# Optimization experiments

Measured on AMD Instinct MI355X. Metric: run time of the kernel, lower is better.

## Reference

```python
import jax, jax.numpy as jnp
import numpy as np
from jax import lax

B, L_IN, D, D_INNER = 4, 1024, 512, 512
H, DK = 8, 64
WIN = [4, 4, 4]
INNER_SIZE = 5   # temporal intra-level neighborhood size
SEM_K = 32       # opt.semantic_node: topk per level for semantic mask
N_LAYER = 2


def _build_temporal_mask(input_size, window_size, inner_size):
    # faithful port of Encoder.get_mask (Pyraformer-Naive mask)
    all_size = [input_size]
    for w in window_size:
        all_size.append(all_size[-1] // w)
    L = sum(all_size)
    m = np.zeros((L, L), dtype=np.float32)
    iw = inner_size // 2
    starts = [sum(all_size[:i]) for i in range(len(all_size))]
    for li, n in enumerate(all_size):
        st = starts[li]
        for i in range(st, st + n):
            m[i, max(i - iw, st):min(i + iw + 1, st + n)] = 1
    for li in range(1, len(all_size)):
        st = starts[li]
        prev = all_size[li - 1]
        w = window_size[li - 1]
        for i in range(st, st + all_size[li]):
            ls = st - prev + (i - st) * w
            rs = st if i == st + all_size[li] - 1 else st - prev + (i - st + 1) * w
            m[i, ls:rs] = 1
            m[ls:rs, i] = 1
    return (1 - m).astype(bool), all_size

TMASK_NP, ALL_SIZE = _build_temporal_mask(L_IN, WIN, INNER_SIZE)
L_TOT = sum(ALL_SIZE)  # 1360


def _ln(x, g, b, eps):
    mu = jnp.mean(x, axis=-1, keepdims=True)
    var = jnp.mean(jnp.square(x - mu), axis=-1, keepdims=True)
    return (x - mu) * lax.rsqrt(var + eps) * g + b


def _mha(x, Wq, Wk, Wv, fcW, fcb, g, b, mask):
    # post-norm MHA (normalize_before=False), dropout disabled (eval)
    Bq, L, _ = x.shape
    q = (x @ Wq).reshape(Bq, L, H, DK)
    k = (x @ Wk).reshape(Bq, L, H, DK)
    v = (x @ Wv).reshape(Bq, L, H, DK)
    a = jnp.einsum('bqhd,bkhd->bhqk', q, k) / np.float32(DK ** 0.5)
    a = jnp.where(mask, -jnp.inf, a)
    p = jax.nn.softmax(a, axis=-1)
    o = jnp.einsum('bhqk,bkhd->bqhd', p, v).reshape(Bq, L, H * DK)
    return _ln(o @ fcW + fcb + x, g, b, 1e-6)


def _semantic_mask(x):
    # get_semantic_mask: per-level cosine similarity, mask topk-most-similar within each level
    nrm = jnp.linalg.norm(x, axis=-1, keepdims=True)
    xn = x / jnp.maximum(nrm, 1e-8)
    sim = jnp.einsum('bid,bjd->bij', xn, xn)
    Bq = x.shape[0]
    mask = jnp.zeros((Bq, L_TOT, L_TOT), dtype=bool)
    bidx = jnp.arange(Bq)[:, None, None]
    start = 0
    for n in ALL_SIZE:
        k = min(n, SEM_K)
        blk = sim[:, start:start + n, start:start + n]
        idx = lax.top_k(blk, k)[1]              # [B, n, k]
        ridx = jnp.arange(n)[None, :, None]
        bm = jnp.zeros((Bq, n, n), dtype=bool).at[bidx, ridx, idx].set(True)
        mask = mask.at[:, start:start + n, start:start + n].set(bm)
        start += n
    return mask


def _bottleneck(x, dW, db, cW, cb, uW, ub, g, b):
    t = jnp.transpose(x @ dW + db, (0, 2, 1))  # [B, d_inner, L]
    outs = []
    for i in range(len(WIN)):
        t = lax.conv_general_dilated(t, cW[i], (WIN[i],), 'VALID',
                                     dimension_numbers=('NCH', 'OIH', 'NCH')) + cb[i][None, :, None]
        t = t / np.float32(np.sqrt(1.0 + 1e-5))  # eval BatchNorm with identity running stats
        t = jax.nn.elu(t)
        outs.append(t)
    pyr = jnp.transpose(jnp.concatenate(outs, axis=2), (0, 2, 1)) @ uW + ub
    return _ln(jnp.concatenate([x, pyr], axis=1), g, b, 1e-5)


def _forward(x_enc, down_W, down_b, conv_W, conv_b, up_W, up_b, bc_ln_g, bc_ln_b,
             attn_Wq, attn_Wk, attn_Wv, attn_fcW, attn_fcb, attn_ln_g, attn_ln_b,
             ffn_W1, ffn_b1, ffn_W2, ffn_b2, ffn_ln_g, ffn_ln_b):
    tmask = jnp.asarray(TMASK_NP)[None, None]  # [1,1,Lt,Lt]
    x = _bottleneck(x_enc, down_W, down_b, conv_W, conv_b, up_W, up_b, bc_ln_g, bc_ln_b)
    for l in range(N_LAYER):
        res = x
        t_out = _mha(x, attn_Wq[l, 0], attn_Wk[l, 0], attn_Wv[l, 0], attn_fcW[l, 0],
                     attn_fcb[l, 0], attn_ln_g[l, 0], attn_ln_b[l, 0], tmask)
        smask = _semantic_mask(x)[:, None]     # [B,1,Lt,Lt]
        s_out = _mha(x, attn_Wq[l, 1], attn_Wk[l, 1], attn_Wv[l, 1], attn_fcW[l, 1],
                     attn_fcb[l, 1], attn_ln_g[l, 1], attn_ln_b[l, 1], smask)
        x = (t_out + s_out + res) / 3.0
        res = x
        h = jax.nn.relu(x @ ffn_W1[l] + ffn_b1[l])
        x = _ln(h @ ffn_W2[l] + ffn_b2[l] + res, ffn_ln_g[l], ffn_ln_b[l], 1e-6)
    return x


def setup_inputs() -> dict:
    key = jax.random.key(0)
    ks = jax.random.split(key, 16)
    s = 0.02
    inp = {
        'x_enc': jax.random.normal(ks[0], (B, L_IN, D), jnp.float32),
        'down_W': jax.random.normal(ks[1], (D, D_INNER), jnp.float32) * s,
        'down_b': jnp.zeros((D_INNER,), jnp.float32),
        'conv_W': jax.random.normal(ks[2], (3, D_INNER, D_INNER, WIN[0]), jnp.float32) * s,
        'conv_b': jnp.zeros((3, D_INNER), jnp.float32),
        'up_W': jax.random.normal(ks[3], (D_INNER, D), jnp.float32) * s,
        'up_b': jnp.zeros((D,), jnp.float32),
        'bc_ln_g': jnp.ones((D,), jnp.float32),
        'bc_ln_b': jnp.zeros((D,), jnp.float32),
        'attn_Wq': jax.random.normal(ks[4], (N_LAYER, 2, D, H * DK), jnp.float32) * s,
        'attn_Wk': jax.random.normal(ks[5], (N_LAYER, 2, D, H * DK), jnp.float32) * s,
        'attn_Wv': jax.random.normal(ks[6], (N_LAYER, 2, D, H * DK), jnp.float32) * s,
        'attn_fcW': jax.random.normal(ks[7], (N_LAYER, 2, H * DK, D), jnp.float32) * s,
        'attn_fcb': jnp.zeros((N_LAYER, 2, D), jnp.float32),
        'attn_ln_g': jnp.ones((N_LAYER, 2, D), jnp.float32),
        'attn_ln_b': jnp.zeros((N_LAYER, 2, D), jnp.float32),
        'ffn_W1': jax.random.normal(ks[8], (N_LAYER, D, D_INNER), jnp.float32) * s,
        'ffn_b1': jnp.zeros((N_LAYER, D_INNER), jnp.float32),
        'ffn_W2': jax.random.normal(ks[9], (N_LAYER, D_INNER, D), jnp.float32) * s,
        'ffn_b2': jnp.zeros((N_LAYER, D), jnp.float32),
        'ffn_ln_g': jnp.ones((N_LAYER, D), jnp.float32),
        'ffn_ln_b': jnp.zeros((N_LAYER, D), jnp.float32),
    }
    return inp


def reference(x_enc, down_W, down_b, conv_W, conv_b, up_W, up_b, bc_ln_g, bc_ln_b,
              attn_Wq, attn_Wk, attn_Wv, attn_fcW, attn_fcb, attn_ln_g, attn_ln_b,
              ffn_W1, ffn_b1, ffn_W2, ffn_b2, ffn_ln_g, ffn_ln_b):
    return _forward(x_enc, down_W, down_b, conv_W, conv_b, up_W, up_b, bc_ln_g, bc_ln_b,
                    attn_Wq, attn_Wk, attn_Wv, attn_fcW, attn_fcb, attn_ln_g, attn_ln_b,
                    ffn_W1, ffn_b1, ffn_W2, ffn_b2, ffn_ln_g, ffn_ln_b)
```

## Files before the change

### kernel.cpp

```cpp
#include <hip/hip_runtime.h>
#include <float.h>
#include <math.h>
#include <stdint.h>

#define LT 1360
#define BB 4
#define DM 512
#define NHH 8
#define NBLE 2785280
#define MBW 24
#define QSCALE 0.18033688f

typedef __attribute__((ext_vector_type(8))) short short8;
typedef __attribute__((ext_vector_type(4))) float f32x4;
typedef unsigned long long u64;

__device__ __forceinline__ ushort f2b(float x){
    uint32_t u = __float_as_uint(x);
    return (ushort)((u + 0x7fffu + ((u >> 16) & 1u)) >> 16);
}
__device__ __forceinline__ float b2f(ushort u){
    return __uint_as_float(((uint32_t)u) << 16);
}
__device__ __forceinline__ float ex2(float x){
    float r;
    asm("v_exp_f32 %0, %1" : "=v"(r) : "v"(x));
    return r;
}
__device__ __forceinline__ uint32_t pkbf(float lo, float hi){
    uint32_t r;
    asm("v_cvt_pk_bf16_f32 %0, %1, %2" : "=v"(r) : "v"(lo), "v"(hi));
    return r;
}

#define SG0 0
#define SG1 1048576
#define SG2 (SG1 + 65536)
#define SG3 (SG2 + 4096)
#define SBT (SG3 + 256)

__device__ __forceinline__ void blk_info(int i, int& bi, int& st, int& n){
    if (i < 1024){ bi = 0; st = 0;    n = 1024; }
    else if (i < 1280){ bi = 1; st = 1024; n = 256; }
    else if (i < 1344){ bi = 2; st = 1280; n = 64; }
    else { bi = 3; st = 1344; n = 16; }
}

__global__ __launch_bounds__(256)
void build_tidx(int* __restrict__ idx, int* __restrict__ cnt){
    int i = blockIdx.x * 256 + threadIdx.x;
    if (i >= LT) return;
    int bi, st, n; blk_info(i, bi, st, n);
    int c = 0; int* row = idx + i * 12;
    int lo = (i - 2 > st) ? i - 2 : st;
    int hi = (i + 2 < st + n - 1) ? i + 2 : st + n - 1;
    for (int j = lo; j <= hi; j++) row[c++] = j;
    if (bi < 3) row[c++] = st + n + (i - st) / 4;
    if (bi > 0){
        int stc = st - n * 4;
        int base = stc + (i - st) * 4;
        for (int t = 0; t < 4; t++) row[c++] = base + t;
    }
    cnt[i] = c;
    for (int t = c; t < 12; t++) row[t] = 0;
}

__global__ __launch_bounds__(256)
void wtrans(const float* __restrict__ W, ushort* __restrict__ Wt, int K, int N, long dstStride){
    int mat = blockIdx.z;
    const float* Ws = W + (size_t)mat * K * N;
    ushort* Wd = Wt + (size_t)mat * dstStride;
    int k0 = blockIdx.y << 6, n0 = blockIdx.x << 6;
    __shared__ ushort t[64][72];
    int tid = threadIdx.x;
    #pragma unroll
    for (int p = 0; p < 4; p++){
        int idx = tid + (p << 8);
        int r = idx >> 4, c4 = (idx & 15) << 2;
        float4 v = *(const float4*)(Ws + (size_t)(k0 + r) * N + n0 + c4);
        t[c4+0][r] = f2b(v.x); t[c4+1][r] = f2b(v.y);
        t[c4+2][r] = f2b(v.z); t[c4+3][r] = f2b(v.w);
    }
    __syncthreads();
    #pragma unroll
    for (int p = 0; p < 4; p++){
        int idx = tid + (p << 8);
        int r = idx >> 4, c4 = (idx & 15) << 2;
        *(uint2*)&Wd[(size_t)(n0 + r) * K + k0 + c4] = *(uint2*)&t[r][c4];
    }
}

__global__ __launch_bounds__(256)
void wconv(const float* __restrict__ cw, ushort* __restrict__ wt){
    int conv = blockIdx.y;
    const float* src = cw + (size_t)conv * 512 * 512 * 4;
    ushort* dst = wt + (size_t)conv * 2048 * 512;
    int idx = blockIdx.x * 256 + threadIdx.x;
    int o = idx >> 11, rest = idx & 2047;
    int k = rest >> 9, ii = rest & 511;
    dst[idx] = f2b(src[((size_t)(o << 9) + ii) * 4 + k]);
}

__global__ __launch_bounds__(256)
void gemm_qkv(const ushort* __restrict__ A, const ushort* __restrict__ Bw,
              void* __restrict__ Cout, int M, int N, int K)
{
    __shared__ ushort As[64][72];
    __shared__ ushort Bs[128][72];
    int tid = threadIdx.x;
    int lane = tid & 63, w = tid >> 6, quad = lane >> 4, l15 = lane & 15;
    int gm = blockIdx.y << 6, gn = blockIdx.x << 7;
    int arow = tid >> 2, ac = (tid & 3) << 4;
    int brow = tid >> 1, bc = (tid & 1) << 5;
    f32x4 acc[4][2];
    #pragma unroll
    for (int mi = 0; mi < 4; mi++)
        #pragma unroll
        for (int ni = 0; ni < 2; ni++)
            acc[mi][ni] = (f32x4){0.f,0.f,0.f,0.f};
    const ushort* Ap = A + (size_t)(gm + arow) * K + ac;
    const ushort* Bp = Bw + (size_t)(gn + brow) * K + bc;
    uint4 a0r = *(const uint4*)(Ap);
    uint4 a1r = *(const uint4*)(Ap + 8);
    uint4 b0r = *(const uint4*)(Bp);
    uint4 b1r = *(const uint4*)(Bp + 8);
    uint4 b2r = *(const uint4*)(Bp + 16);
    uint4 b3r = *(const uint4*)(Bp + 24);
    *(uint4*)&As[arow][ac]     = a0r;  *(uint4*)&As[arow][ac + 8]  = a1r;
    *(uint4*)&Bs[brow][bc]     = b0r;  *(uint4*)&Bs[brow][bc + 8]  = b1r;
    *(uint4*)&Bs[brow][bc + 16] = b2r; *(uint4*)&Bs[brow][bc + 24] = b3r;
    __syncthreads();
    for (int k0 = 0; k0 < K; k0 += 64){
        bool nx = (k0 + 64 < K);
        if (nx){
            a0r = *(const uint4*)(Ap + k0 + 64);
            a1r = *(const uint4*)(Ap + k0 + 72);
            b0r = *(const uint4*)(Bp + k0 + 64);
            b1r = *(const uint4*)(Bp + k0 + 72);
            b2r = *(const uint4*)(Bp + k0 + 80);
            b3r = *(const uint4*)(Bp + k0 + 88);
        }
        __builtin_amdgcn_s_setprio(1);
        #pragma unroll
        for (int kk = 0; kk < 2; kk++){
            short8 af[4], bf[2];
            #pragma unroll
            for (int mi = 0; mi < 4; mi++)
                af[mi] = *(const short8*)&As[(mi << 4) + l15][(kk << 5) + (quad << 3)];
            #pragma unroll
            for (int ni = 0; ni < 2; ni++)
                bf[ni] = *(const short8*)&Bs[(w << 5) + (ni << 4) + l15][(kk << 5) + (quad << 3)];
            #pragma unroll
            for (int mi = 0; mi < 4; mi++)
                #pragma unroll
                for (int ni = 0; ni < 2; ni++)
                    acc[mi][ni] = __builtin_amdgcn_mfma_f32_16x16x32_bf16(af[mi], bf[ni], acc[mi][ni], 0, 0, 0);
        }
        __builtin_amdgcn_s_setprio(0);
        if (nx){
            __syncthreads();
            *(uint4*)&As[arow][ac]     = a0r;  *(uint4*)&As[arow][ac + 8]  = a1r;
            *(uint4*)&Bs[brow][bc]     = b0r;  *(uint4*)&Bs[brow][bc + 8]  = b1r;
            *(uint4*)&Bs[brow][bc + 16] = b2r; *(uint4*)&Bs[brow][bc + 24] = b3r;
            __syncthreads();
        }
    }
    int seg = gn >> 9, gc = gn & 511;
    ushort* Ob = (ushort*)Cout;
    if (seg == 0){
        #pragma unroll
        for (int mi = 0; mi < 4; mi++)
            #pragma unroll
            for (int r = 0; r < 4; r++){
                int row = gm + (mi << 4) + (quad << 2) + r;
                #pragma unroll
                for (int ni = 0; ni < 2; ni++){
                    int c5 = gc + (w << 5) + (ni << 4) + l15;
                    Ob[(size_t)row * 512 + c5] = f2b(acc[mi][ni][r] * QSCALE);
                }
            }
    } else if (seg == 1){
        #pragma unroll
        for (int mi = 0; mi < 4; mi++)
            #pragma unroll
            for (int r = 0; r < 4; r++){
                int row = gm + (mi << 4) + (quad << 2) + r;
                #pragma unroll
                for (int ni = 0; ni < 2; ni++){
                    int c5 = gc + (w << 5) + (ni << 4) + l15;
                    Ob[(size_t)2*NBLE + (size_t)row * 512 + c5] = f2b(acc[mi][ni][r]);
                }
            }
    } else {
        __syncthreads();
        #pragma unroll
        for (int mi = 0; mi < 4; mi++)
            #pragma unroll
            for (int r = 0; r < 4; r++){
                int rloc = (mi << 4) + (quad << 2) + r;
                int row = gm + rloc;
                #pragma unroll
                for (int ni = 0; ni < 2; ni++){
                    int cloc = (w << 5) + (ni << 4) + l15;
                    ushort hv = f2b(acc[mi][ni][r]);
                    Ob[(size_t)5*NBLE + (size_t)row * 512 + gc + cloc] = hv;
                    Bs[cloc][rloc] = hv;
                }
            }
        __syncthreads();
        int colw = tid >> 3;
        int jo = (tid & 7) << 3;
        int rr = gm + jo;
        int bb = rr / LT;
        int ii = rr - bb * LT;
        #pragma unroll
        for (int cc = 0; cc < 4; cc++){
            int c = colw + (cc << 5);
            uint4 tv = *(const uint4*)&Bs[c][jo];
            ushort* dst = Ob + (size_t)4*NBLE + ((size_t)(bb * 512 + gc + c)) * LT + ii;
            *(uint4*)dst = tv;
        }
    }
}

template<int ABF>
__global__ __launch_bounds__(256)
void gemm64t(const void* __restrict__ Avp, const ushort* __restrict__ Bw,
             const float* __restrict__ bias, const float* __restrict__ Rres,
             void* __restrict__ Cout, int M, int N, int K,
             int act, int omode, int mpb, int orpb, int ooff)
{
    __shared__ ushort As[64][72];
    __shared__ ushort Bs[64][72];
    int tid = threadIdx.x;
    int lane = tid & 63, w = tid >> 6, quad = lane >> 4, l15 = lane & 15;
    int gm = blockIdx.y << 6, gn = blockIdx.x << 6;
    int wr = (w >> 1) << 5, wc = (w & 1) << 5;
    int srow = tid >> 2, sc = (tid & 3) << 4;
    f32x4 acc[2][2];
    #pragma unroll
    for (int mi = 0; mi < 2; mi++)
        #pragma unroll
        for (int ni = 0; ni < 2; ni++)
            acc[mi][ni] = (f32x4){0.f,0.f,0.f,0.f};
    const float*  Af = (const float*)Avp;
    const ushort* Ab = (const ushort*)Avp;
    size_t aoff = (size_t)(gm + srow) * K + sc;
    const ushort* Bp = Bw + (size_t)(gn + srow) * K + sc;
    uint4 aR0, aR1, bR0, bR1;
    float4 f0, f1, f2v, f3v;
    if (ABF){
        aR0 = *(const uint4*)(Ab + aoff);
        aR1 = *(const uint4*)(Ab + aoff + 8);
    } else {
        f0  = *(const float4*)(Af + aoff);
        f1  = *(const float4*)(Af + aoff + 4);
        f2v = *(const float4*)(Af + aoff + 8);
        f3v = *(const float4*)(Af + aoff + 12);
    }
    bR0 = *(const uint4*)(Bp);
    bR1 = *(const uint4*)(Bp + 8);
    if (!ABF){
        aR0.x = (uint32_t)f2b(f0.x)  | ((uint32_t)f2b(f0.y)  << 16);
        aR0.y = (uint32_t)f2b(f0.z)  | ((uint32_t)f2b(f0.w)  << 16);
        aR0.z = (uint32_t)f2b(f1.x)  | ((uint32_t)f2b(f1.y)  << 16);
        aR0.w = (uint32_t)f2b(f1.z)  | ((uint32_t)f2b(f1.w)  << 16);
        aR1.x = (uint32_t)f2b(f2v.x) | ((uint32_t)f2b(f2v.y) << 16);
        aR1.y = (uint32_t)f2b(f2v.z) | ((uint32_t)f2b(f2v.w) << 16);
        aR1.z = (uint32_t)f2b(f3v.x) | ((uint32_t)f2b(f3v.y) << 16);
        aR1.w = (uint32_t)f2b(f3v.z) | ((uint32_t)f2b(f3v.w) << 16);
    }
    *(uint4*)&As[srow][sc]     = aR0;
    *(uint4*)&As[srow][sc + 8] = aR1;
    *(uint4*)&Bs[srow][sc]     = bR0;
    *(uint4*)&Bs[srow][sc + 8] = bR1;
    __syncthreads();
    for (int k0 = 0; k0 < K; k0 += 64){
        bool nx = (k0 + 64 < K);
        if (nx){
            if (ABF){
                aR0 = *(const uint4*)(Ab + aoff + k0 + 64);
                aR1 = *(const uint4*)(Ab + aoff + k0 + 72);
            } else {
                f0  = *(const float4*)(Af + aoff + k0 + 64);
                f1  = *(const float4*)(Af + aoff + k0 + 68);
                f2v = *(const float4*)(Af + aoff + k0 + 72);
                f3v = *(const float4*)(Af + aoff + k0 + 76);
            }
            bR0 = *(const uint4*)(Bp + k0 + 64);
            bR1 = *(const uint4*)(Bp + k0 + 72);
        }
        __builtin_amdgcn_s_setprio(1);
        #pragma unroll
        for (int kk = 0; kk < 2; kk++){
            short8 af0 = *(const short8*)&As[wr + l15][(kk << 5) + (quad << 3)];
            short8 af1 = *(const short8*)&As[wr + 16 + l15][(kk << 5) + (quad << 3)];
            short8 bf0 = *(const short8*)&Bs[wc + l15][(kk << 5) + (quad << 3)];
            short8 bf1 = *(const short8*)&Bs[wc + 16 + l15][(kk << 5) + (quad << 3)];
            acc[0][0] = __builtin_amdgcn_mfma_f32_16x16x32_bf16(af0, bf0, acc[0][0], 0, 0, 0);
            acc[0][1] = __builtin_amdgcn_mfma_f32_16x16x32_bf16(af0, bf1, acc[0][1], 0, 0, 0);
            acc[1][0] = __builtin_amdgcn_mfma_f32_16x16x32_bf16(af1, bf0, acc[1][0], 0, 0, 0);
            acc[1][1] = __builtin_amdgcn_mfma_f32_16x16x32_bf16(af1, bf1, acc[1][1], 0, 0, 0);
        }
        __builtin_amdgcn_s_setprio(0);
        if (nx){
            __syncthreads();
            if (!ABF){
                aR0.x = (uint32_t)f2b(f0.x)  | ((uint32_t)f2b(f0.y)  << 16);
                aR0.y = (uint32_t)f2b(f0.z)  | ((uint32_t)f2b(f0.w)  << 16);
                aR0.z = (uint32_t)f2b(f1.x)  | ((uint32_t)f2b(f1.y)  << 16);
                aR0.w = (uint32_t)f2b(f1.z)  | ((uint32_t)f2b(f1.w)  << 16);
                aR1.x = (uint32_t)f2b(f2v.x) | ((uint32_t)f2b(f2v.y) << 16);
                aR1.y = (uint32_t)f2b(f2v.z) | ((uint32_t)f2b(f2v.w) << 16);
                aR1.z = (uint32_t)f2b(f3v.x) | ((uint32_t)f2b(f3v.y) << 16);
                aR1.w = (uint32_t)f2b(f3v.z) | ((uint32_t)f2b(f3v.w) << 16);
            }
            *(uint4*)&As[srow][sc]     = aR0;
            *(uint4*)&As[srow][sc + 8] = aR1;
            *(uint4*)&Bs[srow][sc]     = bR0;
            *(uint4*)&Bs[srow][sc + 8] = bR1;
            __syncthreads();
        }
    }
    #pragma unroll
    for (int mi = 0; mi < 2; mi++){
        #pragma unroll
        for (int r = 0; r < 4; r++){
            int row = gm + wr + (mi << 4) + (quad << 2) + r;
            #pragma unroll
            for (int ni = 0; ni < 2; ni++){
                int col = gn + wc + (ni << 4) + l15;
                float v = acc[mi][ni][r];
                if (bias) v += bias[col];
                if (Rres) v += Rres[(size_t)row * N + col];
                if (act == 2){ v = fmaxf(v, 0.f); }
                if (omode == 0){
                    int orow = mpb ? (row / mpb) * orpb + ooff + (row % mpb) : row;
                    ((float*)Cout)[(size_t)orow * N + col] = v;
                } else {
                    ((ushort*)Cout)[(size_t)row * N + col] = f2b(v);
                }
            }
        }
    }
}

__global__ __launch_bounds__(256)
void gemm_sk(const float* __restrict__ A, const ushort* __restrict__ Bw,
             float* __restrict__ P, int M, int N, int K, int kslice)
{
    __shared__ ushort As[64][40];
    __shared__ ushort Bs[64][40];
    int tid = threadIdx.x;
    int lane = tid & 63, w = tid >> 6, quad = lane >> 4, l15 = lane & 15;
    int gm = blockIdx.y << 6, gn = blockIdx.x << 6;
    int wr = (w >> 1) << 5, wc = (w & 1) << 5;
    int srow = tid >> 2, sc8 = (tid & 3) << 3;
    int ks = blockIdx.z * kslice;
    f32x4 acc[2][2];
    #pragma unroll
    for (int mi = 0; mi < 2; mi++)
        #pragma unroll
        for (int ni = 0; ni < 2; ni++)
            acc[mi][ni] = (f32x4){0.f,0.f,0.f,0.f};
    const float* Ap = A + (size_t)(gm + srow) * K;
    const ushort* Bp = Bw + (size_t)(gn + srow) * K;
    for (int k0 = ks; k0 < ks + kslice; k0 += 32){
        float4 a0 = *(const float4*)(Ap + k0 + sc8);
        float4 a1 = *(const float4*)(Ap + k0 + sc8 + 4);
        uint4 av;
        av.x = (uint32_t)f2b(a0.x) | ((uint32_t)f2b(a0.y) << 16);
        av.y = (uint32_t)f2b(a0.z) | ((uint32_t)f2b(a0.w) << 16);
        av.z = (uint32_t)f2b(a1.x) | ((uint32_t)f2b(a1.y) << 16);
        av.w = (uint32_t)f2b(a1.z) | ((uint32_t)f2b(a1.w) << 16);
        *(uint4*)&As[srow][sc8] = av;
        *(uint4*)&Bs[srow][sc8] = *(const uint4*)(Bp + k0 + sc8);
        __syncthreads();
        short8 af0 = *(const short8*)&As[wr + l15][quad << 3];
        short8 af1 = *(const short8*)&As[wr + 16 + l15][quad << 3];
        short8 bf0 = *(const short8*)&Bs[wc + l15][quad << 3];
        short8 bf1 = *(const short8*)&Bs[wc + 16 + l15][quad << 3];
        acc[0][0] = __builtin_amdgcn_mfma_f32_16x16x32_bf16(af0, bf0, acc[0][0], 0, 0, 0);
        acc[0][1] = __builtin_amdgcn_mfma_f32_16x16x32_bf16(af0, bf1, acc[0][1], 0, 0, 0);
        acc[1][0] = __builtin_amdgcn_mfma_f32_16x16x32_bf16(af1, bf0, acc[1][0], 0, 0, 0);
        acc[1][1] = __builtin_amdgcn_mfma_f32_16x16x32_bf16(af1, bf1, acc[1][1], 0, 0, 0);
        __syncthreads();
    }
    float* Pz = P + (size_t)blockIdx.z * M * N;
    #pragma unroll
    for (int mi = 0; mi < 2; mi++){
        #pragma unroll
        for (int r = 0; r < 4; r++){
            int row = gm + wr + (mi << 4) + (quad << 2) + r;
            #pragma unroll
            for (int ni = 0; ni < 2; ni++){
                int col = gn + wc + (ni << 4) + l15;
                Pz[(size_t)row * N + col] = acc[mi][ni][r];
            }
        }
    }
}

__global__ __launch_bounds__(256)
void sk_reduce(const float* __restrict__ P, const float* __restrict__ bias,
               float* __restrict__ C, int MN, int S)
{
    int idx = (blockIdx.x * 256 + threadIdx.x) << 2;
    if (idx >= MN) return;
    float4 s = {0.f, 0.f, 0.f, 0.f};
    for (int z = 0; z < S; z++){
        float4 v = *(const float4*)(P + (size_t)z * MN + idx);
        s.x += v.x; s.y += v.y; s.z += v.z; s.w += v.w;
    }
    const float cscale = 0.9999950000375f;
    int col = idx & 511;
    float o[4] = {s.x, s.y, s.z, s.w};
    #pragma unroll
    for (int t = 0; t < 4; t++){
        float v = (o[t] + bias[col + t]) * cscale;
        o[t] = (v > 0.f) ? v : expm1f(v);
    }
    *(float4*)(C + idx) = (float4){o[0], o[1], o[2], o[3]};
}

__global__ __launch_bounds__(256)
void sim_mfma(const ushort* __restrict__ XH, const ushort* __restrict__ XL,
              float* __restrict__ SIM){
    __shared__ ushort Ah[64][40], Al[64][40], Bh[64][40], Bl[64][40];
    int x = blockIdx.x, b = blockIdx.y;
    int ti, tj, st, n, goff;
    if (x < 256){ ti = x >> 4; tj = x & 15; st = 0; n = 1024; goff = SG0; }
    else if (x < 272){ int y = x - 256; ti = y >> 2; tj = y & 3; st = 1024; n = 256; goff = SG1; }
    else if (x == 272){ ti = 0; tj = 0; st = 1280; n = 64; goff = SG2; }
    else { ti = 0; tj = 0; st = 1344; n = 16; goff = SG3; }
    const ushort* XbH = XH + (((size_t)b * LT + st) << 9);
    const ushort* XbL = XL + (((size_t)b * LT + st) << 9);
    float* Cb = SIM + (size_t)b * SBT + goff;
    int gm = ti << 6, gn = tj << 6;
    int tid = threadIdx.x;
    int lane = tid & 63, w = tid >> 6, quad = lane >> 4, l15 = lane & 15;
    int wr = (w >> 1) << 5, wc = (w & 1) << 5;
    int srow = tid >> 2, sc8 = (tid & 3) << 3;
    int ra = gm + srow; if (ra > n - 1) ra = n - 1;
    int rb = gn + srow; if (rb > n - 1) rb = n - 1;
    f32x4 acc[2][2];
    #pragma unroll
    for (int mi = 0; mi < 2; mi++)
        #pragma unroll
        for (int ni = 0; ni < 2; ni++)
            acc[mi][ni] = (f32x4){0.f,0.f,0.f,0.f};
    const ushort* pAh = XbH + ((size_t)ra << 9) + sc8;
    const ushort* pAl = XbL + ((size_t)ra << 9) + sc8;
    const ushort* pBh = XbH + ((size_t)rb << 9) + sc8;
    const ushort* pBl = XbL + ((size_t)rb << 9) + sc8;
    uint4 vah = *(const uint4*)pAh;
    uint4 val = *(const uint4*)pAl;
    uint4 vbh = *(const uint4*)pBh;
    uint4 vbl = *(const uint4*)pBl;
    *(uint4*)&Ah[srow][sc8] = vah;
    *(uint4*)&Al[srow][sc8] = val;
    *(uint4*)&Bh[srow][sc8] = vbh;
    *(uint4*)&Bl[srow][sc8] = vbl;
    __syncthreads();
    for (int k0 = 0; k0 < 512; k0 += 32){
        bool nx = (k0 + 32 < 512);
        if (nx){
            vah = *(const uint4*)(pAh + k0 + 32);
            val = *(const uint4*)(pAl + k0 + 32);
            vbh = *(const uint4*)(pBh + k0 + 32);
            vbl = *(const uint4*)(pBl + k0 + 32);
        }
        __builtin_amdgcn_s_setprio(1);
        short8 ah0 = *(const short8*)&Ah[wr + l15][quad << 3];
        short8 ah1 = *(const short8*)&Ah[wr + 16 + l15][quad << 3];
        short8 al0 = *(const short8*)&Al[wr + l15][quad << 3];
        short8 al1 = *(const short8*)&Al[wr + 16 + l15][quad << 3];
        short8 bh0 = *(const short8*)&Bh[wc + l15][quad << 3];
        short8 bh1 = *(const short8*)&Bh[wc + 16 + l15][quad << 3];
        short8 bl0 = *(const short8*)&Bl[wc + l15][quad << 3];
        short8 bl1 = *(const short8*)&Bl[wc + 16 + l15][quad << 3];
        acc[0][0] = __builtin_amdgcn_mfma_f32_16x16x32_bf16(ah0, bh0, acc[0][0], 0, 0, 0);
        acc[0][0] = __builtin_amdgcn_mfma_f32_16x16x32_bf16(ah0, bl0, acc[0][0], 0, 0, 0);
        acc[0][0] = __builtin_amdgcn_mfma_f32_16x16x32_bf16(al0, bh0, acc[0][0], 0, 0, 0);
        acc[0][1] = __builtin_amdgcn_mfma_f32_16x16x32_bf16(ah0, bh1, acc[0][1], 0, 0, 0);
        acc[0][1] = __builtin_amdgcn_mfma_f32_16x16x32_bf16(ah0, bl1, acc[0][1], 0, 0, 0);
        acc[0][1] = __builtin_amdgcn_mfma_f32_16x16x32_bf16(al0, bh1, acc[0][1], 0, 0, 0);
        acc[1][0] = __builtin_amdgcn_mfma_f32_16x16x32_bf16(ah1, bh0, acc[1][0], 0, 0, 0);
        acc[1][0] = __builtin_amdgcn_mfma_f32_16x16x32_bf16(ah1, bl0, acc[1][0], 0, 0, 0);
        acc[1][0] = __builtin_amdgcn_mfma_f32_16x16x32_bf16(al1, bh0, acc[1][0], 0, 0, 0);
        acc[1][1] = __builtin_amdgcn_mfma_f32_16x16x32_bf16(ah1, bh1, acc[1][1], 0, 0, 0);
        acc[1][1] = __builtin_amdgcn_mfma_f32_16x16x32_bf16(ah1, bl1, acc[1][1], 0, 0, 0);
        acc[1][1] = __builtin_amdgcn_mfma_f32_16x16x32_bf16(al1, bh1, acc[1][1], 0, 0, 0);
        __builtin_amdgcn_s_setprio(0);
        if (nx){
            __syncthreads();
            *(uint4*)&Ah[srow][sc8] = vah;
            *(uint4*)&Al[srow][sc8] = val;
            *(uint4*)&Bh[srow][sc8] = vbh;
            *(uint4*)&Bl[srow][sc8] = vbl;
            __syncthreads();
        }
    }
    #pragma unroll
    for (int mi = 0; mi < 2; mi++){
        #pragma unroll
        for (int r = 0; r < 4; r++){
            int row = gm + wr + (mi << 4) + (quad << 2) + r;
            if (row < n){
                #pragma unroll
                for (int ni = 0; ni < 2; ni++){
                    int col = gn + wc + (ni << 4) + l15;
                    if (col < n) Cb[(size_t)row * n + col] = acc[mi][ni][r];
                }
            }
        }
    }
}

__global__ __launch_bounds__(256)
void pcat_copy(const float* __restrict__ C1, const float* __restrict__ C2,
               const float* __restrict__ C3, float* __restrict__ PC){
    int idx = blockIdx.x * 256 + threadIdx.x;
    int d = idx & 511;
    int r = (idx >> 9) % 336;
    int b = idx / (336 * 512);
    float v;
    if (r < 256)       v = C1[(((size_t)b * 256 + r) << 9) + d];
    else if (r < 320)  v = C2[(((size_t)b * 64 + (r - 256)) << 9) + d];
    else               v = C3[(((size_t)b * 16 + (r - 320)) << 9) + d];
    PC[idx] = v;
}

__global__ __launch_bounds__(256)
void xenc_copy(const float* __restrict__ xe, float* __restrict__ dst){
    int idx = blockIdx.x * 256 + threadIdx.x;
    int d = idx & 511;
    int l = (idx >> 9) & 1023;
    int b = idx >> 19;
    dst[(((size_t)b * LT + l) << 9) + d] = xe[idx];
}

__global__ __launch_bounds__(256)
void ln_kernel(const float* __restrict__ in, const float* __restrict__ g,
               const float* __restrict__ bta, float* __restrict__ out,
               ushort* __restrict__ ob, float eps){
    int wid = threadIdx.x >> 6, lane = threadIdx.x & 63;
    int row = blockIdx.x * 4 + wid;
    const float* p = in + ((size_t)row << 9);
    float vals[8]; float s = 0.f, s2 = 0.f;
    #pragma unroll
    for (int t = 0; t < 8; t++){
        float v = p[lane + t * 64]; vals[t] = v; s += v; s2 += v * v;
    }
    #pragma unroll
    for (int off = 32; off; off >>= 1){
        s  += __shfl_xor(s,  off, 64);
        s2 += __shfl_xor(s2, off, 64);
    }
    float mu = s * (1.f / 512.f);
    float var = s2 * (1.f / 512.f) - mu * mu;
    float r = rsqrtf(var + eps);
    float* q = out + ((size_t)row << 9);
    ushort* qb = ob ? ob + ((size_t)row << 9) : nullptr;
    #pragma unroll
    for (int t = 0; t < 8; t++){
        int c = lane + t * 64;
        float v = (vals[t] - mu) * r * g[c] + bta[c];
        q[c] = v;
        if (qb) qb[c] = f2b(v);
    }
}

__global__ __launch_bounds__(256)
void ln_add3(const float* __restrict__ in, const float* __restrict__ g,
             const float* __restrict__ bta, const float* __restrict__ T,
             float* __restrict__ X, ushort* __restrict__ ob, float eps){
    int wid = threadIdx.x >> 6, lane = threadIdx.x & 63;
    int row = blockIdx.x * 4 + wid;
    const float* p = in + ((size_t)row << 9);
    float vals[8]; float s = 0.f, s2 = 0.f;
    #pragma unroll
    for (int t = 0; t < 8; t++){
        float v = p[lane + t * 64]; vals[t] = v; s += v; s2 += v * v;
    }
    #pragma unroll
    for (int off = 32; off; off >>= 1){
        s  += __shfl_xor(s,  off, 64);
        s2 += __shfl_xor(s2, off, 64);
    }
    float mu = s * (1.f / 512.f);
    float var = s2 * (1.f / 512.f) - mu * mu;
    float r = rsqrtf(var + eps);
    const float* tp = T + ((size_t)row << 9);
    float* xp = X + ((size_t)row << 9);
    ushort* qb = ob + ((size_t)row << 9);
    #pragma unroll
    for (int t = 0; t < 8; t++){
        int c = lane + t * 64;
        float sn = (vals[t] - mu) * r * g[c] + bta[c];
        float nv = (tp[c] + sn + xp[c]) * (1.f / 3.f);
        xp[c] = nv;
        qb[c] = f2b(nv);
    }
}

__global__ __launch_bounds__(256)
void rownorm_kernel(const float* __restrict__ in, ushort* __restrict__ XHp,
                    ushort* __restrict__ XLp){
    int wid = threadIdx.x >> 6, lane = threadIdx.x & 63;
    int row = blockIdx.x * 4 + wid;
    const float* p = in + ((size_t)row << 9);
    float vals[8]; float s2 = 0.f;
    #pragma unroll
    for (int t = 0; t < 8; t++){
        float v = p[lane + t * 64]; vals[t] = v; s2 += v * v;
    }
    #pragma unroll
    for (int off = 32; off; off >>= 1) s2 += __shfl_xor(s2, off, 64);
    float inv = 1.f / fmaxf(sqrtf(s2), 1e-8f);
    ushort* qh = XHp + ((size_t)row << 9);
    ushort* ql = XLp + ((size_t)row << 9);
    #pragma unroll
    for (int t = 0; t < 8; t++){
        float v = vals[t] * inv;
        ushort h = f2b(v);
        qh[lane + t * 64] = h;
        ql[lane + t * 64] = f2b(v - b2f(h));
    }
}

__global__ __launch_bounds__(256)
void topk_sel(const float* __restrict__ SIM, u64* __restrict__ MB){
    int wid = threadIdx.x >> 6, lane = threadIdx.x & 63;
    int r = blockIdx.x * 4 + wid;
    int b = r / LT, i = r % LT;
    int bi, st, n; blk_info(i, bi, st, n);
    u64* mrow = MB + ((size_t)b * LT + i) * MBW;
    if (n == 16){
        u64 myw = 0;
        if (lane == 21) myw = ~0ULL;
        if (lane < MBW) mrow[lane] = myw;
        return;
    }
    int goff = (bi == 0) ? SG0 : (bi == 1) ? SG1 : SG2;
    const float* srow = SIM + (size_t)b * SBT + goff + (size_t)(i - st) * n;
    int ns = n >> 6;
    float vals[16];
    #pragma unroll
    for (int t = 0; t < 16; t++)
        vals[t] = (t < ns) ? srow[lane + (t << 6)] : -FLT_MAX;

    float c[32];
    #pragma unroll
    for (int t = 0; t < 16; t++) c[t] = vals[t];
    #pragma unroll
    for (int k = 2; k <= 16; k <<= 1){
        #pragma unroll
        for (int j = k >> 1; j > 0; j >>= 1){
            #pragma unroll
            for (int t = 0; t < 16; t++){
                int l = t ^ j;
                if (l > t){
                    float lo = fminf(c[t], c[l]);
                    float hi = fmaxf(c[t], c[l]);
                    if ((t & k) == 0){ c[t] = hi; c[l] = lo; }
                    else             { c[t] = lo; c[l] = hi; }
                }
            }
        }
    }
    #pragma unroll
    for (int t = 16; t < 32; t++) c[t] = -FLT_MAX;

    float V32;
    #pragma unroll
    for (int rd = 0; rd < 6; rd++){
        float f[32];
        #pragma unroll
        for (int t = 0; t < 32; t++) f[t] = __shfl_xor(c[t], 1 << rd, 64);
        float m[32];
        #pragma unroll
        for (int t = 0; t < 32; t++) m[t] = fmaxf(c[t], f[31 - t]);
        if (rd < 5){
            #pragma unroll
            for (int d = 16; d >= 1; d >>= 1){
                #pragma unroll
                for (int t = 0; t < 32; t++){
                    if ((t & d) == 0){
                        float lo = fminf(m[t], m[t + d]);
                        m[t] = fmaxf(m[t], m[t + d]);
                        m[t + d] = lo;
                    }
                }
            }
            #pragma unroll
            for (int t = 0; t < 32; t++) c[t] = m[t];
        } else {
            float mn = m[0];
            #pragma unroll
            for (int t = 1; t < 32; t++) mn = fminf(mn, m[t]);
            V32 = mn;
        }
    }

    int cnt_gt = 0;
    #pragma unroll
    for (int t = 0; t < 16; t++){
        u64 bg = __ballot(vals[t] > V32);
        cnt_gt += __popcll(bg);
    }
    int need = 32 - cnt_gt;
    u64 lmask = (1ULL << lane) - 1;
    u64 myw = 0;
    if (lane == 21) myw = 0xFFFFFFFFFFFF0000ULL;
    int eqrun = 0;
    int w0 = st >> 6;
    #pragma unroll
    for (int t = 0; t < 16; t++){
        bool eq = (vals[t] == V32);
        u64 beq = __ballot(eq);
        int below = __popcll(beq & lmask);
        bool sel = (vals[t] > V32) || (eq && (eqrun + below) < need);
        eqrun += __popcll(beq);
        u64 wsel = __ballot(sel);
        if (t < ns && lane == w0 + t) myw = wsel;
    }
    if (lane < MBW) mrow[lane] = myw;
}

__global__ __launch_bounds__(256)
void attn_sparse(const ushort* __restrict__ Q, const ushort* __restrict__ Kp,
                 const ushort* __restrict__ Vn, const int* __restrict__ IDX,
                 const int* __restrict__ CNT, ushort* __restrict__ O){
    int wid = threadIdx.x >> 6, lane = threadIdx.x & 63;
    int row = blockIdx.x * 4 + wid;
    int b = row / (NHH * LT);
    int rem = row % (NHH * LT);
    int h = rem / LT, i = rem % LT;
    int c = CNT[i];
    int jl = IDX[i * 12 + (lane % 12)];
    float qd = b2f(Q[(((size_t)b * LT + i) << 9) + h * 64 + lane]);
    const ushort* kb = Kp + (((size_t)b * LT) << 9) + h * 64 + lane;
    const ushort* vb = Vn + (((size_t)b * LT) << 9) + h * 64 + lane;
    int jj[12];
    #pragma unroll
    for (int t = 0; t < 12; t++) jj[t] = __shfl(jl, t, 64);
    float kv[12], vv[12];
    #pragma unroll
    for (int t = 0; t < 12; t++){
        kv[t] = b2f(kb[(size_t)jj[t] << 9]);
        vv[t] = b2f(vb[(size_t)jj[t] << 9]);
    }
    float lsum = 0.f, o = 0.f;
// ... 61 lines not shown
        uint4 kn0, kn1, vn0, vn1;
        if (havenext){
            kn0 = *(const uint4*)kpp;
            kn1 = *(const uint4*)(kpp + 8);
            vn0 = *(const uint4*)vpp;
            vn1 = *(const uint4*)(vpp + 8);
            kpp += 64 * 512; vpp += 64;
        }
        u64 mw = mpp[kt];
        f32x4 s[4];
        #pragma unroll
        for (int nt = 0; nt < 4; nt++) s[nt] = (f32x4){0.f,0.f,0.f,0.f};
        __builtin_amdgcn_s_setprio(1);
        #pragma unroll
        for (int nt = 0; nt < 4; nt++){
            short8 kf0 = *(const short8*)&Ks[cur][(nt << 4) + l15][quad << 3];
            short8 kf1 = *(const short8*)&Ks[cur][(nt << 4) + l15][32 + (quad << 3)];
            s[nt] = __builtin_amdgcn_mfma_f32_16x16x32_bf16(kf0, qf0, s[nt], 0, 0, 0);
            s[nt] = __builtin_amdgcn_mfma_f32_16x16x32_bf16(kf1, qf1, s[nt], 0, 0, 0);
        }
        __builtin_amdgcn_s_setprio(0);
        u64 msh = mw >> (quad << 2);
        uint32_t pk01[4], pk23[4];
        #pragma unroll
        for (int nt = 0; nt < 4; nt++){
            float p0 = ((uint32_t)(msh >> (nt * 16 + 0)) & 1u) ? 0.f : ex2(s[nt][0]);
            float p1 = ((uint32_t)(msh >> (nt * 16 + 1)) & 1u) ? 0.f : ex2(s[nt][1]);
            float p2 = ((uint32_t)(msh >> (nt * 16 + 2)) & 1u) ? 0.f : ex2(s[nt][2]);
            float p3 = ((uint32_t)(msh >> (nt * 16 + 3)) & 1u) ? 0.f : ex2(s[nt][3]);
            l_part += (p0 + p1) + (p2 + p3);
            pk01[nt] = pkbf(p0, p1);
            pk23[nt] = pkbf(p2, p3);
        }
        uint4 pa, pb;
        {
            uint32_t t0, t1;
            t0 = __shfl(pk01[0], srcA, 64); t1 = __shfl(pk01[1], srcA, 64);
            pa.x = ntHi ? t1 : t0;
            t0 = __shfl(pk23[0], srcA, 64); t1 = __shfl(pk23[1], srcA, 64);
            pa.y = ntHi ? t1 : t0;
            t0 = __shfl(pk01[0], srcB, 64); t1 = __shfl(pk01[1], srcB, 64);
            pa.z = ntHi ? t1 : t0;
            t0 = __shfl(pk23[0], srcB, 64); t1 = __shfl(pk23[1], srcB, 64);
            pa.w = ntHi ? t1 : t0;
            t0 = __shfl(pk01[2], srcA, 64); t1 = __shfl(pk01[3], srcA, 64);
            pb.x = ntHi ? t1 : t0;
            t0 = __shfl(pk23[2], srcA, 64); t1 = __shfl(pk23[3], srcA, 64);
            pb.y = ntHi ? t1 : t0;
            t0 = __shfl(pk01[2], srcB, 64); t1 = __shfl(pk01[3], srcB, 64);
            pb.z = ntHi ? t1 : t0;
            t0 = __shfl(pk23[2], srcB, 64); t1 = __shfl(pk23[3], srcB, 64);
            pb.w = ntHi ? t1 : t0;
        }
        short8 pf0 = *(const short8*)&pa;
        short8 pf1 = *(const short8*)&pb;
        __builtin_amdgcn_s_setprio(1);
        #pragma unroll
        for (int dt = 0; dt < 4; dt++){
            short8 vf0 = *(const short8*)&Vs[cur][(dt << 4) + l15][quad << 3];
            short8 vf1 = *(const short8*)&Vs[cur][(dt << 4) + l15][32 + (quad << 3)];
            Oacc[dt] = __builtin_amdgcn_mfma_f32_16x16x32_bf16(pf0, vf0, Oacc[dt], 0, 0, 0);
            Oacc[dt] = __builtin_amdgcn_mfma_f32_16x16x32_bf16(pf1, vf1, Oacc[dt], 0, 0, 0);
        }
        __builtin_amdgcn_s_setprio(0);
        if (havenext){
            int nb = cur ^ 1;
            *(uint4*)&Ks[nb][srow][sc]     = kn0;
            *(uint4*)&Ks[nb][srow][sc + 8] = kn1;
            *(uint4*)&Vs[nb][srow][sc]     = vn0;
            *(uint4*)&Vs[nb][srow][sc + 8] = vn1;
        }
        __syncthreads();
    }
    l_part += __shfl_xor(l_part, 16, 64);
    l_part += __shfl_xor(l_part, 32, 64);
    #pragma unroll
    for (int r = 0; r < 4; r++){
        int qrow = q0 + (w << 4) + (quad << 2) + r;
        if (qrow < LT){
            float lr = __shfl(l_part, (lane & 48) + (quad << 2) + r, 64);
            float inv = 1.f / lr;
            #pragma unroll
            for (int dt = 0; dt < 4; dt++)
                AO[((size_t)(b * LT + qrow) << 9) + h * 64 + (dt << 4) + l15] =
                    f2b(Oacc[dt][r] * inv);
        }
    }
}

extern "C" void kernel_launch(void* const* d_in, const int* in_sizes, int n_in,
                              void* d_out, int out_size, void* d_ws, size_t ws_size,
                              hipStream_t stream)
{
    const float* x_enc   = (const float*)d_in[0];
    const float* down_W  = (const float*)d_in[1];
    const float* down_b  = (const float*)d_in[2];
    const float* conv_W  = (const float*)d_in[3];
    const float* conv_b  = (const float*)d_in[4];
    const float* up_W    = (const float*)d_in[5];
    const float* up_b    = (const float*)d_in[6];
    const float* bc_g    = (const float*)d_in[7];
    const float* bc_b    = (const float*)d_in[8];
    const float* aWq     = (const float*)d_in[9];
    const float* aWk     = (const float*)d_in[10];
    const float* aWv     = (const float*)d_in[11];
    const float* afcW    = (const float*)d_in[12];
    const float* afcb    = (const float*)d_in[13];
    const float* alng    = (const float*)d_in[14];
    const float* alnb    = (const float*)d_in[15];
    const float* fW1     = (const float*)d_in[16];
    const float* fb1     = (const float*)d_in[17];
    const float* fW2     = (const float*)d_in[18];
    const float* fb2     = (const float*)d_in[19];
    const float* flng    = (const float*)d_in[20];
    const float* flnb    = (const float*)d_in[21];

    const size_t NBL = (size_t)NBLE;
    float* X   = (float*)d_ws;
    float* TMP = X   + NBL;
    float* Qb  = TMP + NBL;
    float* Kb  = Qb  + NBL;
    float* Vb  = Kb  + NBL;
    float* AO  = Vb  + NBL;
    float* TO  = AO  + NBL;
    float* SO  = TO  + NBL;
    u64* MBm = (u64*)(SO + NBL);
    int* TIDX = (int*)(MBm + (size_t)BB * LT * MBW);
    int* TCNT = TIDX + (size_t)LT * 12;
    ushort* WG = (ushort*)(TCNT + LT);
    const size_t M512 = 262144;
    ushort* WdownT = WG;                 size_t wo = M512;
    ushort* WupT   = WG + wo;            wo += M512;
    ushort* Wqkv   = WG + wo;            wo += 12 * M512;
    ushort* WfT    = WG + wo;            wo += 4 * M512;
    ushort* W1T    = WG + wo;            wo += 2 * M512;
    ushort* W2T    = WG + wo;            wo += 2 * M512;
    ushort* WCt    = WG + wo;            wo += 3 * 1048576;
    float* LP = (float*)(WG + wo);
    (void)LP;
    size_t need = 8 * NBL * sizeof(float) + (size_t)BB * LT * MBW * 8
                + (size_t)LT * 13 * 4 + wo * sizeof(ushort)
                + (size_t)2 * BB * NHH * LT * 4;
    if (ws_size < need) return;

    float* Y    = Qb;
    float* C1   = Kb;
    float* C2   = C1 + (size_t)BB*256*512;
    float* C3   = C2 + (size_t)BB*64*512;
    float* PCAT = Vb;
    float* SKP  = AO;
    ushort* XNh = (ushort*)AO;
    ushort* XNl = XNh + NBLE;
    float* SIMB = Qb;
    ushort* QbH = (ushort*)Qb;
    ushort* KbH = (ushort*)Kb;
    ushort* VtH = (ushort*)Vb;
    ushort* VnH = VtH + NBLE;
    ushort* XB  = (ushort*)SO;
    ushort* AOb = (ushort*)AO;
    ushort* HfB = (ushort*)Qb;

    auto gemmN = [&](const void* A, int abf, const ushort* Bw, const float* bias,
                     const float* res, void* C, int M,
                     int act, int omode, int mpb, int orpb, int ooff){
        dim3 grid(8, M / 64);
        if (abf) gemm64t<1><<<grid, 256, 0, stream>>>(A, Bw, bias, res, C, M, 512, 512,
                                                      act, omode, mpb, orpb, ooff);
        else     gemm64t<0><<<grid, 256, 0, stream>>>(A, Bw, bias, res, C, M, 512, 512,
                                                      act, omode, mpb, orpb, ooff);
    };
    auto convG = [&](const float* A, const ushort* Bw, const float* bias,
                     float* C, int M){
        const int S = 8, K = 2048, N = 512;
        gemm_sk<<<dim3(8, M / 64, S), 256, 0, stream>>>(A, Bw, SKP, M, N, K, K / S);
        sk_reduce<<<(M * N) / 1024, 256, 0, stream>>>(SKP, bias, C, M * N, S);
    };

    build_tidx<<<(LT + 255) / 256, 256, 0, stream>>>(TIDX, TCNT);
    wtrans<<<dim3(8, 8, 1), 256, 0, stream>>>(down_W, WdownT, 512, 512, M512);
    wtrans<<<dim3(8, 8, 1), 256, 0, stream>>>(up_W,   WupT,   512, 512, M512);
    wtrans<<<dim3(8, 8, 4), 256, 0, stream>>>(aWq,  Wqkv + 0 * M512, 512, 512, 3 * (long)M512);
    wtrans<<<dim3(8, 8, 4), 256, 0, stream>>>(aWk,  Wqkv + 1 * M512, 512, 512, 3 * (long)M512);
    wtrans<<<dim3(8, 8, 4), 256, 0, stream>>>(aWv,  Wqkv + 2 * M512, 512, 512, 3 * (long)M512);
    wtrans<<<dim3(8, 8, 4), 256, 0, stream>>>(afcW, WfT, 512, 512, M512);
    wtrans<<<dim3(8, 8, 2), 256, 0, stream>>>(fW1,  W1T, 512, 512, M512);
    wtrans<<<dim3(8, 8, 2), 256, 0, stream>>>(fW2,  W2T, 512, 512, M512);
    wconv<<<dim3(4096, 3), 256, 0, stream>>>(conv_W, WCt);

    gemmN(x_enc, 0, WdownT, down_b, nullptr, Y, BB*1024, 0, 0, 0, 0, 0);
    convG(Y,  WCt,             conv_b + 0,    C1, BB*256);
    convG(C1, WCt + 1048576,   conv_b + 512,  C2, BB*64);
    convG(C2, WCt + 2*1048576, conv_b + 1024, C3, BB*16);
    pcat_copy<<<(BB*336*512)/256, 256, 0, stream>>>(C1, C2, C3, PCAT);
    gemmN(PCAT, 0, WupT, up_b, nullptr, TMP, BB*336, 0, 0, 336, LT, 1024);
    xenc_copy<<<(BB*1024*512)/256, 256, 0, stream>>>(x_enc, TMP);
    ln_kernel<<<(BB*LT)/4, 256, 0, stream>>>(TMP, bc_g, bc_b, X, XB, 1e-5f);

    for (int l = 0; l < 2; l++){
        rownorm_kernel<<<(BB*LT)/4, 256, 0, stream>>>(X, XNh, XNl);
        sim_mfma<<<dim3(274, BB), 256, 0, stream>>>(XNh, XNl, SIMB);
        topk_sel<<<(BB*LT)/4, 256, 0, stream>>>(SIMB, MBm);

        for (int j = 0; j < 2; j++){
            int li = l * 2 + j;
            const float* bf = afcb + (size_t)li * 512;
            const float* lg = alng + (size_t)li * 512;
            const float* lb = alnb + (size_t)li * 512;
            gemm_qkv<<<dim3(12, 85), 256, 0, stream>>>(XB, Wqkv + (size_t)li * 3 * M512,
                                                       QbH, BB*LT, 1536, 512);
            if (j == 0){
                attn_sparse<<<(BB*NHH*LT)/4, 256, 0, stream>>>(QbH, KbH, VnH, TIDX, TCNT, AOb);
            } else {
                flash_mfma<<<dim3(32, 22), 256, 0, stream>>>(QbH, KbH, VtH, MBm, AOb);
            }
            gemmN(AOb, 1, WfT + (size_t)li * M512, bf, X, TMP, BB*LT, 0, 0, 0, 0, 0);
            if (j == 0)
                ln_kernel<<<(BB*LT)/4, 256, 0, stream>>>(TMP, lg, lb, TO, nullptr, 1e-6f);
            else
                ln_add3<<<(BB*LT)/4, 256, 0, stream>>>(TMP, lg, lb, TO, X, XB, 1e-6f);
        }

        gemmN(XB,  1, W1T + (size_t)l * M512, fb1 + (size_t)l*512, nullptr, HfB, BB*LT, 2, 1, 0, 0, 0);
        gemmN(HfB, 1, W2T + (size_t)l * M512, fb2 + (size_t)l*512, X, TMP, BB*LT, 0, 0, 0, 0, 0);
        ln_kernel<<<(BB*LT)/4, 256, 0, stream>>>(TMP, flng + (size_t)l*512, flnb + (size_t)l*512,
                                                 (l == 1) ? (float*)d_out : X,
                                                 (l == 1) ? nullptr : XB, 1e-6f);
    }
}
```

Before: 810.6 us.

## Batch both attention branches: merged QKV GEMM, dual fc GEMM, fused dual LayerNorm

Both attention sub-layers read the same input X, so the change computes Q/K/V for both in one wide GEMM with N=3072 and six output segments. It then runs the sparse and flash attentions back to back and does both output projections in a single launch using grid z=2. A new ln2_add3 kernel normalizes both branch outputs and averages them with X in one pass. This cuts the number of kernel launches and fills the GPU with larger grids, at the cost of more scratch memory. It assumes the buffer layout (U offsets, TO reused as TMP1) does not alias anything still live.

```diff
diff --git a/kernel.cpp b/kernel.cpp
--- a/kernel.cpp
+++ b/kernel.cpp
@@ -167,7 +167,7 @@
     }
     int seg = gn >> 9, gc = gn & 511;
     ushort* Ob = (ushort*)Cout;
-    if (seg == 0){
+    if (seg == 2){
         #pragma unroll
         for (int mi = 0; mi < 4; mi++)
             #pragma unroll
@@ -175,36 +175,21 @@
                 int row = gm + (mi << 4) + (quad << 2) + r;
                 #pragma unroll
                 for (int ni = 0; ni < 2; ni++){
-                    int c5 = gc + (w << 5) + (ni << 4) + l15;
-                    Ob[(size_t)row * 512 + c5] = f2b(acc[mi][ni][r] * QSCALE);
+                    int cloc = (w << 5) + (ni << 4) + l15;
+                    Ob[(size_t)5*NBLE + (size_t)row * 512 + gc + cloc] = f2b(acc[mi][ni][r]);
                 }
             }
-    } else if (seg == 1){
-        #pragma unroll
-        for (int mi = 0; mi < 4; mi++)
-            #pragma unroll
-            for (int r = 0; r < 4; r++){
-                int row = gm + (mi << 4) + (quad << 2) + r;
-                #pragma unroll
-                for (int ni = 0; ni < 2; ni++){
-                    int c5 = gc + (w << 5) + (ni << 4) + l15;
-                    Ob[(size_t)2*NBLE + (size_t)row * 512 + c5] = f2b(acc[mi][ni][r]);
-                }
-            }
-    } else {
+    } else if (seg == 5){
         __syncthreads();
         #pragma unroll
         for (int mi = 0; mi < 4; mi++)
             #pragma unroll
             for (int r = 0; r < 4; r++){
                 int rloc = (mi << 4) + (quad << 2) + r;
-                int row = gm + rloc;
                 #pragma unroll
                 for (int ni = 0; ni < 2; ni++){
                     int cloc = (w << 5) + (ni << 4) + l15;
-                    ushort hv = f2b(acc[mi][ni][r]);
-                    Ob[(size_t)5*NBLE + (size_t)row * 512 + gc + cloc] = hv;
-                    Bs[cloc][rloc] = hv;
+                    Bs[cloc][rloc] = f2b(acc[mi][ni][r]);
                 }
             }
         __syncthreads();
@@ -220,6 +205,21 @@
             ushort* dst = Ob + (size_t)4*NBLE + ((size_t)(bb * 512 + gc + c)) * LT + ii;
             *(uint4*)dst = tv;
         }
+    } else {
+        size_t base = (seg == 0) ? 0 : (seg == 1) ? (size_t)2*NBLE
+                    : (seg == 3) ? (size_t)NBLE : (size_t)3*NBLE;
+        float scl = (seg == 0 || seg == 3) ? QSCALE : 1.f;
+        #pragma unroll
+        for (int mi = 0; mi < 4; mi++)
+            #pragma unroll
+            for (int r = 0; r < 4; r++){
+                int row = gm + (mi << 4) + (quad << 2) + r;
+                #pragma unroll
+                for (int ni = 0; ni < 2; ni++){
+                    int c5 = gc + (w << 5) + (ni << 4) + l15;
+                    Ob[base + (size_t)row * 512 + c5] = f2b(acc[mi][ni][r] * scl);
+                }
+            }
     }
 }
 
@@ -340,6 +340,86 @@
                 } else {
                     ((ushort*)Cout)[(size_t)row * N + col] = f2b(v);
                 }
+            }
+        }
+    }
+}
+
+__global__ __launch_bounds__(256)
+void gemm_fc2(const ushort* __restrict__ A0, const ushort* __restrict__ A1,
+              const ushort* __restrict__ B0, const ushort* __restrict__ B1,
+              const float* __restrict__ bias0, const float* __restrict__ bias1,
+              const float* __restrict__ Rres, float* __restrict__ C0,
+              float* __restrict__ C1, int M, int N, int K)
+{
+    __shared__ ushort As[64][72];
+    __shared__ ushort Bs[64][72];
+    const ushort* Ab = blockIdx.z ? A1 : A0;
+    const ushort* Bw = blockIdx.z ? B1 : B0;
+    const float* bias = blockIdx.z ? bias1 : bias0;
+    float* Cout = blockIdx.z ? C1 : C0;
+    int tid = threadIdx.x;
+    int lane = tid & 63, w = tid >> 6, quad = lane >> 4, l15 = lane & 15;
+    int gm = blockIdx.y << 6, gn = blockIdx.x << 6;
+    int wr = (w >> 1) << 5, wc = (w & 1) << 5;
+    int srow = tid >> 2, sc = (tid & 3) << 4;
+    f32x4 acc[2][2];
+    #pragma unroll
+    for (int mi = 0; mi < 2; mi++)
+        #pragma unroll
+        for (int ni = 0; ni < 2; ni++)
+            acc[mi][ni] = (f32x4){0.f,0.f,0.f,0.f};
+    size_t aoff = (size_t)(gm + srow) * K + sc;
+    const ushort* Bp = Bw + (size_t)(gn + srow) * K + sc;
+    uint4 aR0 = *(const uint4*)(Ab + aoff);
+    uint4 aR1 = *(const uint4*)(Ab + aoff + 8);
+    uint4 bR0 = *(const uint4*)(Bp);
+    uint4 bR1 = *(const uint4*)(Bp + 8);
+    *(uint4*)&As[srow][sc]     = aR0;
+    *(uint4*)&As[srow][sc + 8] = aR1;
+    *(uint4*)&Bs[srow][sc]     = bR0;
+    *(uint4*)&Bs[srow][sc + 8] = bR1;
+    __syncthreads();
+    for (int k0 = 0; k0 < K; k0 += 64){
+        bool nx = (k0 + 64 < K);
+        if (nx){
+            aR0 = *(const uint4*)(Ab + aoff + k0 + 64);
+            aR1 = *(const uint4*)(Ab + aoff + k0 + 72);
+            bR0 = *(const uint4*)(Bp + k0 + 64);
+            bR1 = *(const uint4*)(Bp + k0 + 72);
+        }
+        __builtin_amdgcn_s_setprio(1);
+        #pragma unroll
+        for (int kk = 0; kk < 2; kk++){
+            short8 af0 = *(const short8*)&As[wr + l15][(kk << 5) + (quad << 3)];
+            short8 af1 = *(const short8*)&As[wr + 16 + l15][(kk << 5) + (quad << 3)];
+            short8 bf0 = *(const short8*)&Bs[wc + l15][(kk << 5) + (quad << 3)];
+            short8 bf1 = *(const short8*)&Bs[wc + 16 + l15][(kk << 5) + (quad << 3)];
+            acc[0][0] = __builtin_amdgcn_mfma_f32_16x16x32_bf16(af0, bf0, acc[0][0], 0, 0, 0);
+            acc[0][1] = __builtin_amdgcn_mfma_f32_16x16x32_bf16(af0, bf1, acc[0][1], 0, 0, 0);
+            acc[1][0] = __builtin_amdgcn_mfma_f32_16x16x32_bf16(af1, bf0, acc[1][0], 0, 0, 0);
+            acc[1][1] = __builtin_amdgcn_mfma_f32_16x16x32_bf16(af1, bf1, acc[1][1], 0, 0, 0);
+        }
+        __builtin_amdgcn_s_setprio(0);
+        if (nx){
+            __syncthreads();
+            *(uint4*)&As[srow][sc]     = aR0;
+            *(uint4*)&As[srow][sc + 8] = aR1;
+            *(uint4*)&Bs[srow][sc]     = bR0;
+            *(uint4*)&Bs[srow][sc + 8] = bR1;
+            __syncthreads();
+        }
+    }
+    #pragma unroll
+    for (int mi = 0; mi < 2; mi++){
+        #pragma unroll
+        for (int r = 0; r < 4; r++){
+            int row = gm + wr + (mi << 4) + (quad << 2) + r;
+            #pragma unroll
+            for (int ni = 0; ni < 2; ni++){
+                int col = gn + wc + (ni << 4) + l15;
+                float v = acc[mi][ni][r] + bias[col] + Rres[(size_t)row * N + col];
+                Cout[(size_t)row * N + col] = v;
             }
         }
     }
@@ -572,33 +652,40 @@
 }
 
 __global__ __launch_bounds__(256)
-void ln_add3(const float* __restrict__ in, const float* __restrict__ g,
-             const float* __restrict__ bta, const float* __restrict__ T,
-             float* __restrict__ X, ushort* __restrict__ ob, float eps){
+void ln2_add3(const float* __restrict__ in0, const float* __restrict__ in1,
+              const float* __restrict__ g0, const float* __restrict__ b0,
+              const float* __restrict__ g1, const float* __restrict__ b1,
+              float* __restrict__ X, ushort* __restrict__ ob, float eps){
     int wid = threadIdx.x >> 6, lane = threadIdx.x & 63;
     int row = blockIdx.x * 4 + wid;
-    const float* p = in + ((size_t)row << 9);
-    float vals[8]; float s = 0.f, s2 = 0.f;
+    const float* p0 = in0 + ((size_t)row << 9);
+    const float* p1 = in1 + ((size_t)row << 9);
+    float v0[8], v1[8];
+    float s0 = 0.f, q0 = 0.f, s1 = 0.f, q1 = 0.f;
     #pragma unroll
     for (int t = 0; t < 8; t++){
-        float v = p[lane + t * 64]; vals[t] = v; s += v; s2 += v * v;
+        float a = p0[lane + t * 64]; v0[t] = a; s0 += a; q0 += a * a;
+        float c = p1[lane + t * 64]; v1[t] = c; s1 += c; q1 += c * c;
     }
     #pragma unroll
     for (int off = 32; off; off >>= 1){
-        s  += __shfl_xor(s,  off, 64);
-        s2 += __shfl_xor(s2, off, 64);
-    }
-    float mu = s * (1.f / 512.f);
-    float var = s2 * (1.f / 512.f) - mu * mu;
-    float r = rsqrtf(var + eps);
-    const float* tp = T + ((size_t)row << 9);
+        s0 += __shfl_xor(s0, off, 64);
+        q0 += __shfl_xor(q0, off, 64);
+        s1 += __shfl_xor(s1, off, 64);
+        q1 += __shfl_xor(q1, off, 64);
+    }
+    float mu0 = s0 * (1.f / 512.f);
+    float r0 = rsqrtf(q0 * (1.f / 512.f) - mu0 * mu0 + eps);
+    float mu1 = s1 * (1.f / 512.f);
+    float r1 = rsqrtf(q1 * (1.f / 512.f) - mu1 * mu1 + eps);
     float* xp = X + ((size_t)row << 9);
     ushort* qb = ob + ((size_t)row << 9);
     #pragma unroll
     for (int t = 0; t < 8; t++){
         int c = lane + t * 64;
-        float sn = (vals[t] - mu) * r * g[c] + bta[c];
-        float nv = (tp[c] + sn + xp[c]) * (1.f / 3.f);
+        float sn0 = (v0[t] - mu0) * r0 * g0[c] + b0[c];
+        float sn1 = (v1[t] - mu1) * r1 * g1[c] + b1[c];
+        float nv = (sn0 + sn1 + xp[c]) * (1.f / 3.f);
         xp[c] = nv;
         qb[c] = f2b(nv);
     }
@@ -966,13 +1053,12 @@
     ushort* XNh = (ushort*)AO;
     ushort* XNl = XNh + NBLE;
     float* SIMB = Qb;
-    ushort* QbH = (ushort*)Qb;
-    ushort* KbH = (ushort*)Kb;
-    ushort* VtH = (ushort*)Vb;
-    ushort* VnH = VtH + NBLE;
+    ushort* U   = (ushort*)Qb;
     ushort* XB  = (ushort*)SO;
-    ushort* AOb = (ushort*)AO;
+    ushort* AOb0 = (ushort*)AO;
+    ushort* AOb1 = AOb0 + NBLE;
     ushort* HfB = (ushort*)Qb;
+    float* TMP1 = TO;
 
     auto gemmN = [&](const void* A, int abf, const ushort* Bw, const float* bias,
                      const float* res, void* C, int M,
@@ -1015,24 +1101,20 @@
         sim_mfma<<<dim3(274, BB), 256, 0, stream>>>(XNh, XNl, SIMB);
         topk_sel<<<(BB*LT)/4, 256, 0, stream>>>(SIMB, MBm);
 
-        for (int j = 0; j < 2; j++){
-            int li = l * 2 + j;
-            const float* bf = afcb + (size_t)li * 512;
-            const float* lg = alng + (size_t)li * 512;
-            const float* lb = alnb + (size_t)li * 512;
-            gemm_qkv<<<dim3(12, 85), 256, 0, stream>>>(XB, Wqkv + (size_t)li * 3 * M512,
-                                                       QbH, BB*LT, 1536, 512);
-            if (j == 0){
-                attn_sparse<<<(BB*NHH*LT)/4, 256, 0, stream>>>(QbH, KbH, VnH, TIDX, TCNT, AOb);
-            } else {
-                flash_mfma<<<dim3(32, 22), 256, 0, stream>>>(QbH, KbH, VtH, MBm, AOb);
-            }
-            gemmN(AOb, 1, WfT + (size_t)li * M512, bf, X, TMP, BB*LT, 0, 0, 0, 0, 0);
-            if (j == 0)
-                ln_kernel<<<(BB*LT)/4, 256, 0, stream>>>(TMP, lg, lb, TO, nullptr, 1e-6f);
-            else
-                ln_add3<<<(BB*LT)/4, 256, 0, stream>>>(TMP, lg, lb, TO, X, XB, 1e-6f);
-        }
+        gemm_qkv<<<dim3(24, 85), 256, 0, stream>>>(XB, Wqkv + (size_t)l * 6 * M512,
+                                                   U, BB*LT, 3072, 512);
+        attn_sparse<<<(BB*NHH*LT)/4, 256, 0, stream>>>(U, U + 2*NBL, U + 5*NBL,
+                                                       TIDX, TCNT, AOb0);
+        flash_mfma<<<dim3(32, 22), 256, 0, stream>>>(U + NBL, U + 3*NBL, U + 4*NBL,
+                                                     MBm, AOb1);
+        gemm_fc2<<<dim3(8, 85, 2), 256, 0, stream>>>(AOb0, AOb1,
+            WfT + (size_t)(2*l) * M512, WfT + (size_t)(2*l + 1) * M512,
+            afcb + (size_t)(2*l) * 512, afcb + (size_t)(2*l + 1) * 512,
+            X, TMP, TMP1, BB*LT, 512, 512);
+        ln2_add3<<<(BB*LT)/4, 256, 0, stream>>>(TMP, TMP1,
+            alng + (size_t)(2*l) * 512, alnb + (size_t)(2*l) * 512,
+            alng + (size_t)(2*l + 1) * 512, alnb + (size_t)(2*l + 1) * 512,
+            X, XB, 1e-6f);
 
         gemmN(XB,  1, W1T + (size_t)l * M512, fb1 + (size_t)l*512, nullptr, HfB, BB*LT, 2, 1, 0, 0, 0);
         gemmN(HfB, 1, W2T + (size_t)l * M512, fb2 + (size_t)l*512, X, TMP, BB*LT, 0, 0, 0, 0, 0);
```

After: 732.9 us. -9.6%, faster.
